# Kernel optimization log

Measured on AMD Instinct MI355X. Metric: run time of the kernel, lower is better.

Reference implementation:

```python
import jax, jax.numpy as jnp
import numpy as np
from jax import lax

EPS = 1e-8  # torch CosineSimilarity eps


def setup_inputs() -> dict:
    key = jax.random.key(0)
    k1, k2, k3 = jax.random.split(key, 3)
    B, T, D, K = 16, 2048, 768, 64
    inputs = jax.random.normal(k1, (B, T, D), dtype=jnp.float32)
    labels = jax.random.randint(k2, (B, T), 0, K, dtype=jnp.int64)
    class_avgs = jax.random.normal(k3, (K, D), dtype=jnp.float32)
    return {"inputs": inputs, "labels": labels, "class_avgs": class_avgs}


def _simrel(inputs, labels, class_avgs):
    B, T, D = inputs.shape
    K = class_avgs.shape[0]
    vecs = inputs.reshape(B * T, D)
    labs = labels.reshape(B * T)
    class_ids = jnp.arange(K)

    def step(carry, xl):
        avgs, counts = carry  # [K,D], [K]
        vec, lab = xl  # [D], scalar int
        is_inf = jnp.any(jnp.isinf(avgs), axis=1)  # [K] unseen-class flag
        vn = jnp.maximum(jnp.linalg.norm(vec), EPS)
        an = jnp.maximum(jnp.linalg.norm(avgs, axis=1), EPS)  # [K]
        cos = (avgs @ vec) / (an * vn)  # [K]
        onehot = class_ids == lab
        # unseen class: sim = 1 (cos(vec,vec)) if labeled, else -1
        sim = jnp.where(is_inf, jnp.where(onehot, 1.0, -1.0), cos)
        # training update: running mean of labeled class (counts reset per forward)
        cnt = counts[lab]
        new_row = jnp.where(is_inf[lab], vec, (avgs[lab] * cnt + vec) / (cnt + 1.0))
        avgs = avgs.at[lab].set(new_row)
        counts = counts.at[lab].add(1.0)
        return (avgs, counts), sim

    init = (class_avgs, jnp.zeros((K,), dtype=inputs.dtype))
    (_, _), sims = lax.scan(step, init, (vecs, labs))
    return sims.reshape(B, T, K)


def reference(inputs, labels, class_avgs):
    return _simrel(inputs, labels, class_avgs)
```

## Files before the change

### kernel.cpp

```cpp
#include <hip/hip_runtime.h>
#include <cstddef>

#define K 64
#define D 768
#define D4 192

__device__ __forceinline__ float d4f(float4 a, float4 b) {
  return a.x*b.x + a.y*b.y + a.z*b.z + a.w*b.w;
}
__device__ __forceinline__ float4 a4(float4 a, float4 b) {
  return make_float4(a.x+b.x, a.y+b.y, a.z+b.z, a.w+b.w);
}
__device__ __forceinline__ unsigned short f2bf(float x) {
  unsigned int u = __float_as_uint(x);
  unsigned int r = (u + 0x7FFFu + ((u >> 16) & 1u)) >> 16;
  return (unsigned short)r;
}
__device__ __forceinline__ float bflo(unsigned u) { return __uint_as_float(u << 16); }
__device__ __forceinline__ float bfhi(unsigned u) { return __uint_as_float(u & 0xFFFF0000u); }

typedef __attribute__((ext_vector_type(8)))  short bf16x8;
typedef __attribute__((ext_vector_type(16))) float f32x16;

#define NCF 256
#define CF  128
#define NF  32768

__global__ __launch_bounds__(256) void k1c(
    const float* __restrict__ cavg, unsigned short* __restrict__ cavgb,
    float* __restrict__ cn2)
{
  int wave = blockIdx.x * 4 + (threadIdx.x >> 6);
  int l = threadIdx.x & 63;
  if (wave >= K) return;
  const float* src = cavg + (size_t)wave * D;
  unsigned short* dst = cavgb + (size_t)wave * D;
  float sq = 0.f;
#pragma unroll
  for (int t = 0; t < 3; ++t) {
    float4 v = ((const float4*)src)[t * 64 + l];
    sq += v.x*v.x + v.y*v.y + v.z*v.z + v.w*v.w;
    ushort4 o; o.x = f2bf(v.x); o.y = f2bf(v.y); o.z = f2bf(v.z); o.w = f2bf(v.w);
    ((ushort4*)dst)[t * 64 + l] = o;
  }
#pragma unroll
  for (int m = 1; m <= 32; m <<= 1) sq += __shfl_xor(sq, m);
  if (l == 0) cn2[wave] = sq;
}

#define LDT2 132
#define LDM  136
__global__ __launch_bounds__(256) void k2_v9(
    const float* __restrict__ inputs, const int* __restrict__ labels,
    unsigned short* __restrict__ Vb, unsigned short* __restrict__ sums,
    int* __restrict__ cnts_t)
{
  __shared__ unsigned short Vt[128 * LDT2];
  __shared__ unsigned short Mt[64 * LDM];
  const int bi = blockIdx.x;
  const int m = bi / 6, g = bi % 6;
  const int tid = threadIdx.x;
  const int w = tid >> 6, l = tid & 63;
  const int r31 = l & 31, kh = l >> 5;

  float4 fa[8], fb[8];
#pragma unroll
  for (int it = 0; it < 8; ++it) {
    int flat = it * 256 + tid;
    int row = flat >> 4, c8 = flat & 15;
    const float* src = inputs + (size_t)(m * 128 + row) * D + g * 128 + c8 * 8;
    fa[it] = *(const float4*)src;
    fb[it] = *(const float4*)(src + 4);
  }

  for (int e = tid; e < 64 * LDM / 2; e += 256) ((unsigned int*)Mt)[e] = 0u;
  __syncthreads();
  if (tid < 128) Mt[labels[m * 128 + tid] * LDM + tid] = 0x3F80;
  __syncthreads();
  if (g == 0 && tid < 64) {
    int c = 0;
    for (int j = 0; j < 128; ++j) c += (Mt[tid * LDM + j] != 0);
    cnts_t[tid * NCF + m] = c;
  }

#pragma unroll
  for (int it = 0; it < 8; ++it) {
    int flat = it * 256 + tid;
    int row = flat >> 4, c8 = flat & 15;
    uint4 u;
    u.x = (unsigned)f2bf(fa[it].x) | ((unsigned)f2bf(fa[it].y) << 16);
    u.y = (unsigned)f2bf(fa[it].z) | ((unsigned)f2bf(fa[it].w) << 16);
    u.z = (unsigned)f2bf(fb[it].x) | ((unsigned)f2bf(fb[it].y) << 16);
    u.w = (unsigned)f2bf(fb[it].z) | ((unsigned)f2bf(fb[it].w) << 16);
    *(uint4*)(Vt + row * LDT2 + c8 * 8) = u;
    *(uint4*)(Vb + (size_t)(m * 128 + row) * D + g * 128 + c8 * 8) = u;
  }
  __syncthreads();

  f32x16 acc0 = (f32x16){}, acc1 = (f32x16){};
#pragma unroll
  for (int kk = 0; kk < 8; ++kk) {
    bf16x8 a0 = *(const bf16x8*)(Mt + (r31) * LDM + kk * 16 + kh * 8);
    bf16x8 a1 = *(const bf16x8*)(Mt + (32 + r31) * LDM + kk * 16 + kh * 8);
    bf16x8 b;
#pragma unroll
    for (int r = 0; r < 8; ++r)
      b[r] = *(const short*)(Vt + (kk * 16 + kh * 8 + r) * LDT2 + w * 32 + r31);
    acc0 = __builtin_amdgcn_mfma_f32_32x32x16_bf16(a0, b, acc0, 0, 0, 0);
    acc1 = __builtin_amdgcn_mfma_f32_32x32x16_bf16(a1, b, acc1, 0, 0, 0);
  }

  __syncthreads();
  unsigned short* So = Vt;
#pragma unroll
  for (int q = 0; q < 16; ++q) {
    int kc = (q & 3) + 8 * (q >> 2) + 4 * kh;
    So[kc * 128 + w * 32 + r31]        = f2bf(acc0[q]);
    So[(32 + kc) * 128 + w * 32 + r31] = f2bf(acc1[q]);
  }
  __syncthreads();
  unsigned short* sp = sums + (size_t)m * (K * D) + g * 128;
#pragma unroll
  for (int it = 0; it < 4; ++it) {
    int flat = it * 256 + tid;
    int row = flat >> 4, c = flat & 15;
    *(uint4*)(sp + (size_t)row * D + c * 8) = *(const uint4*)(So + row * 128 + c * 8);
  }
}

__global__ __launch_bounds__(256) void k3a_scan_lo(
    unsigned short* __restrict__ sums, float* __restrict__ aux)
{
  const int g  = blockIdx.x / 96;
  const int cp = (blockIdx.x % 96) * 256 + threadIdx.x;
  const int col = cp * 2;
  float run0 = 0.f, run1 = 0.f;
  for (int m = g * 16; m < g * 16 + 16; ++m) {
    size_t idx = (size_t)m * (K * D) + col;
    unsigned u = *(const unsigned*)(sums + idx);
    float t0 = bflo(u), t1 = bfhi(u);
    *(unsigned*)(sums + idx) = (unsigned)f2bf(run0) | ((unsigned)f2bf(run1) << 16);
    run0 += t0; run1 += t1;
  }
  aux[(size_t)g * (K * D) + col]     = run0;
  aux[(size_t)g * (K * D) + col + 1] = run1;
}

__global__ __launch_bounds__(256) void k3b_plus(
    float* __restrict__ aux, int* __restrict__ cnts_t)
{
  if (blockIdx.x == 192) {
    if (threadIdx.x < K) {
      int k = threadIdx.x;
      int run = 0;
      int* p = cnts_t + k * NCF;
      for (int mm = 0; mm < NCF; ++mm) { int t = p[mm]; p[mm] = run; run += t; }
    }
    return;
  }
  int col = blockIdx.x * 256 + threadIdx.x;
  float run = 0.f;
  for (int g = 0; g < 16; ++g) {
    size_t idx = (size_t)g * (K * D) + col;
    float t = aux[idx]; aux[idx] = run; run += t;
  }
}

#define LDV2 136
#define LDD  132
#define BUFW (2 * 128 * LDV2)
__global__ __launch_bounds__(1024, 4) void k4_v7(
    const unsigned short* __restrict__ Vb, const unsigned short* __restrict__ base,
    const float* __restrict__ aux, const unsigned short* __restrict__ cavgb,
    const int* __restrict__ labels, const int* __restrict__ cnts_t,
    const float* __restrict__ cn2, float* __restrict__ out)
{
  __shared__ unsigned short smem[2 * BUFW];
  __shared__ float pvL[128];
  __shared__ float bn2L[64];
  __shared__ int   labL[128];
  __shared__ float chk[16][64];
  const int m = blockIdx.x;
  const int g = m >> 4;
  const int tid = threadIdx.x;
  const int w = tid >> 6, l = tid & 63;
  const int r31 = l & 31, kh = l >> 5;
  const int wr = w & 3;
  const int wc = w >> 2;

  if (tid < 128) labL[tid] = labels[m * 128 + tid];
  if (tid < 64) bn2L[tid] = 0.f;
  __syncthreads();

  f32x16 accP = (f32x16){}, accS = (f32x16){};

  uint4 vreg[2], breg, creg;
  float4 areg[2];

#define PREF(sx) do {                                                          \
    _Pragma("unroll")                                                          \
    for (int it = 0; it < 2; ++it) {                                           \
      int flat = it * 1024 + tid;                                              \
      int row = flat >> 4, c = flat & 15;                                      \
      vreg[it] = *(const uint4*)(Vb + (size_t)(m * 128 + row) * D + (sx) * 128 + c * 8); \
      if (it == 0) {                                                           \
        breg = *(const uint4*)(base + ((size_t)m * K + row) * D + (sx) * 128 + c * 8); \
        const float* ap = aux + ((size_t)g * K + row) * D + (sx) * 128 + c * 8; \
        areg[0] = *(const float4*)ap;                                          \
        areg[1] = *(const float4*)(ap + 4);                                    \
      } else {                                                                 \
        creg = *(const uint4*)(cavgb + (size_t)(row - 64) * D + (sx) * 128 + c * 8); \
      }                                                                        \
    }                                                                          \
  } while (0)

#define WRITEB(pb) do {                                                        \
    unsigned short* Vt_ = smem + (pb) * BUFW;                                  \
    unsigned short* Bt_ = Vt_ + 128 * LDV2;                                    \
    _Pragma("unroll")                                                          \
    for (int it = 0; it < 2; ++it) {                                           \
      int flat = it * 1024 + tid;                                              \
      int row = flat >> 4, c = flat & 15;                                      \
      *(uint4*)(Vt_ + row * LDV2 + c * 8) = vreg[it];                          \
      if (it == 0) {                                                           \
        uint4 ub = breg;                                                       \
        float4 af0 = areg[0], af1 = areg[1];                                   \
        float f0 = bflo(ub.x) + af0.x, f1 = bfhi(ub.x) + af0.y;                \
        float f2 = bflo(ub.y) + af0.z, f3 = bfhi(ub.y) + af0.w;                \
        float f4 = bflo(ub.z) + af1.x, f5 = bfhi(ub.z) + af1.y;                \
        float f6 = bflo(ub.w) + af1.z, f7 = bfhi(ub.w) + af1.w;                \
        float sq = f0*f0 + f1*f1 + f2*f2 + f3*f3 + f4*f4 + f5*f5 + f6*f6 + f7*f7; \
        sq += __shfl_xor(sq, 1); sq += __shfl_xor(sq, 2);                      \
        sq += __shfl_xor(sq, 4); sq += __shfl_xor(sq, 8);                      \
        if ((l & 15) == 0) atomicAdd(&bn2L[row], sq);                          \
        uint4 u;                                                               \
        u.x = (unsigned)f2bf(f0) | ((unsigned)f2bf(f1) << 16);                 \
        u.y = (unsigned)f2bf(f2) | ((unsigned)f2bf(f3) << 16);                 \
        u.z = (unsigned)f2bf(f4) | ((unsigned)f2bf(f5) << 16);                 \
        u.w = (unsigned)f2bf(f6) | ((unsigned)f2bf(f7) << 16);                 \
        *(uint4*)(Bt_ + row * LDV2 + c * 8) = u;                               \
      } else {                                                                 \
        *(uint4*)(Bt_ + row * LDV2 + c * 8) = creg;                            \
      }                                                                        \
    }                                                                          \
  } while (0)

  PREF(0);
  WRITEB(0);
  PREF(1);
  __syncthreads();

  for (int s = 0; s < 6; ++s) {
    const int pb = s & 1;
    if (s < 5) WRITEB(pb ^ 1);
    if (s < 4) PREF(s + 2);
    const unsigned short* Vt = smem + pb * BUFW;
    const unsigned short* Bt = Vt + 128 * LDV2;
#pragma unroll
    for (int kk = 0; kk < 8; ++kk) {
      bf16x8 av = *(const bf16x8*)(Vt + (32 * wr + r31) * LDV2 + kk * 16 + kh * 8);
      bf16x8 bB = *(const bf16x8*)(Bt + (32 * wc + r31) * LDV2 + kk * 16 + kh * 8);
      accP = __builtin_amdgcn_mfma_f32_32x32x16_bf16(av, bB, accP, 0, 0, 0);
      bf16x8 bV = *(const bf16x8*)(Vt + (32 * wc + r31) * LDV2 + kk * 16 + kh * 8);
      accS = __builtin_amdgcn_mfma_f32_32x32x16_bf16(av, bV, accS, 0, 0, 0);
    }
    __syncthreads();
  }
#undef PREF
#undef WRITEB

  if (wr == wc && ((r31 >> 2) & 1) == kh) {
    int q = (r31 & 3) + 4 * (r31 >> 3);
    pvL[32 * wr + r31] = accS[q];
  }

  {
    unsigned short* Vt = smem;
    unsigned short* Bt = smem + 128 * LDV2;
#pragma unroll
    for (int q = 0; q < 16; ++q) {
      int i = 32 * wr + (q & 3) + 8 * (q >> 2) + 4 * kh;
      int j = 32 * wc + r31;
      Vt[i * LDV2 + j] = (j < i) ? f2bf(accS[q]) : (unsigned short)0;
    }
    int j = tid & 127;
    int lab = labL[j];
    int kb = (tid >> 7) * 8;
#pragma unroll
    for (int kk = 0; kk < 8; ++kk) {
      int k = kb + kk;
      Bt[k * LDV2 + j] = (lab == k) ? (unsigned short)0x3F80 : (unsigned short)0;
    }
  }
  __syncthreads();

  if (w < 8) {
    const unsigned short* Vt = smem;
    const unsigned short* Bt = smem + 128 * LDV2;
#pragma unroll
    for (int kk = 0; kk < 8; ++kk) {
      bf16x8 aS = *(const bf16x8*)(Vt + (32 * wr + r31) * LDV2 + kk * 16 + kh * 8);
      bf16x8 bM = *(const bf16x8*)(Bt + (32 * wc + r31) * LDV2 + kk * 16 + kh * 8);
      accP = __builtin_amdgcn_mfma_f32_32x32x16_bf16(aS, bM, accP, 0, 0, 0);
    }
  }
  __syncthreads();

  float* dotL = (float*)smem;
#pragma unroll
  for (int q = 0; q < 16; ++q) {
    int i = 32 * wr + (q & 3) + 8 * (q >> 2) + 4 * kh;
    dotL[i * LDD + 32 * wc + r31] = accP[q];
  }
  __syncthreads();

  if (w == 0) {
    int k = l;
    bool seen = cnts_t[k * NCF + m] > 0;
    float n = seen ? bn2L[k] : 0.f;
    for (int seg = 0; seg < 16; ++seg) {
      chk[seg][k] = seen ? n : -1.f;
      if (seg == 15) break;
      for (int j = seg * 8; j < seg * 8 + 8; ++j) {
        float dS = dotL[j * LDD + k];
        float pvj = pvL[j];
        if (labL[j] == k) {
          n = seen ? (n + 2.f * dS + pvj) : pvj;
          seen = true;
        }
      }
    }
  }
  __syncthreads();

  {
    int k = l;
    float st = chk[w][k];
    bool seen = st >= 0.f;
    float n = seen ? st : 0.f;
    float cnk = cn2[k];
    int jb = w * 8;
    for (int j = jb; j < jb + 8; ++j) {
      float dS = dotL[j * LDD + k];
      float dC = dotL[j * LDD + 64 + k];
      float pvj = pvL[j];
      int lab = labL[j];
      float val = seen ? dS : dC;
      float nn  = seen ? n : cnk;
      out[(size_t)(m * 128 + j) * K + k] = val * rsqrtf(fmaxf(nn * pvj, 1e-30f));
      if (lab == k) {
        n = seen ? (n + 2.f * dS + pvj) : pvj;
        seen = true;
      }
    }
  }
}

__global__ __launch_bounds__(256) void ph1_chunk_sums(
    const float* __restrict__ inputs, const int* __restrict__ labels,
    float* __restrict__ sums, int* __restrict__ cnts, int NC, int C)
{
  __shared__ float acc[4 * K * 64];
  __shared__ int   hist[4 * K];
  const int bi    = blockIdx.x;
  const int chunk = bi / 12, slice = bi % 12;
  const int w = threadIdx.x >> 6, l = threadIdx.x & 63;

  for (int e = threadIdx.x; e < 4 * K * 64; e += 256) acc[e] = 0.f;
  hist[threadIdx.x] = 0;
  __syncthreads();

  const int C4 = C >> 2;
  const long long rbase = (long long)chunk * C + (long long)w * C4;
  float* accw = acc + w * (K * 64);
  for (int j = 0; j < C4; ++j) {
    long long r = rbase + j;
    int lab = labels[r];
    float v = inputs[r * D + slice * 64 + l];
    accw[lab * 64 + l] += v;
    if (slice == 0 && l == 0) hist[w * K + lab]++;
  }
  __syncthreads();

  float* sp = sums + (long long)chunk * (K * D) + slice * 64;
  for (int e = threadIdx.x; e < K * 64; e += 256) {
    int k = e >> 6, dl = e & 63;
    float s = acc[0*K*64 + e] + acc[1*K*64 + e] + acc[2*K*64 + e] + acc[3*K*64 + e];
    sp[k * D + dl] = s;
  }
  if (slice == 0 && threadIdx.x < K) {
    cnts[chunk * K + threadIdx.x] =
        hist[0*K + threadIdx.x] + hist[1*K + threadIdx.x] +
        hist[2*K + threadIdx.x] + hist[3*K + threadIdx.x];
  }
}

__global__ __launch_bounds__(256) void ph2a_scan_sums(float* __restrict__ sums, int NC)
{
  const int tid = blockIdx.x * 256 + threadIdx.x;
  float run = 0.f;
  for (int m = 0; m < NC; ++m) {
    long long idx = (long long)m * (K * D) + tid;
    float t = sums[idx];
    sums[idx] = run;
    run += t;
  }
}

__global__ void ph2b_scan_cnts(int* __restrict__ cnts, int NC)
{
  const int k = threadIdx.x;
  int run = 0;
  for (int m = 0; m < NC; ++m) {
    int t = cnts[m * K + k];
    cnts[m * K + k] = run;
    run += t;
  }
}

__global__ __launch_bounds__(256, 4) void ph3_scan(
    const float* __restrict__ inputs, const int* __restrict__ labels,
    const float* __restrict__ cavg, const float* __restrict__ base,
    const int* __restrict__ cnts, float* __restrict__ out, int NC, int C)
{
  const int bi = blockIdx.x;
  int chunk, quad;
  if (NC >= 8) {
    int xcd = bi & 7, slot = bi >> 3;
    chunk = xcd * (NC >> 3) + (slot >> 2);
    quad  = slot & 3;
  } else {
    chunk = bi >> 2; quad = bi & 3;
  }
  const int w = threadIdx.x >> 6, l = threadIdx.x & 63;
  const int k0 = (quad * 4 + w) * 4;

  const int cb = chunk * K + k0;
  bool vg0 = (cnts[cb+0] == 0), vg1 = (cnts[cb+1] == 0);
  bool vg2 = (cnts[cb+2] == 0), vg3 = (cnts[cb+3] == 0);

  const float4* bp = (const float4*)base + (long long)chunk * (K * D4);
  const float4* cp = (const float4*)cavg;

  float4 A0[3], A1[3], A2[3], A3[3];
#pragma unroll
  for (int t = 0; t < 3; ++t) {
    int o = t * 64 + l;
    A0[t] = vg0 ? cp[(k0+0)*D4 + o] : bp[(k0+0)*D4 + o];
    A1[t] = vg1 ? cp[(k0+1)*D4 + o] : bp[(k0+1)*D4 + o];
    A2[t] = vg2 ? cp[(k0+2)*D4 + o] : bp[(k0+2)*D4 + o];
    A3[t] = vg3 ? cp[(k0+3)*D4 + o] : bp[(k0+3)*D4 + o];
  }
  float n0 = 0.f, n1 = 0.f, n2 = 0.f, n3 = 0.f;
#pragma unroll
  for (int t = 0; t < 3; ++t) {
    n0 += d4f(A0[t], A0[t]); n1 += d4f(A1[t], A1[t]);
    n2 += d4f(A2[t], A2[t]); n3 += d4f(A3[t], A3[t]);
  }
#pragma unroll
  for (int m = 1; m <= 32; m <<= 1) {
    n0 += __shfl_xor(n0, m); n1 += __shfl_xor(n1, m);
    n2 += __shfl_xor(n2, m); n3 += __shfl_xor(n3, m);
  }

  const long long ibase = (long long)chunk * C;
  for (int j = 0; j < C; ++j) {
    const long long i = ibase + j;
    const int lab = labels[i];
    const float4* vp = (const float4*)inputs + i * D4;
    float4 v0 = vp[l], v1 = vp[64 + l], v2 = vp[128 + l];

    float p0 = d4f(A0[0], v0) + d4f(A0[1], v1) + d4f(A0[2], v2);
    float p1 = d4f(A1[0], v0) + d4f(A1[1], v1) + d4f(A1[2], v2);
    float p2 = d4f(A2[0], v0) + d4f(A2[1], v1) + d4f(A2[2], v2);
    float p3 = d4f(A3[0], v0) + d4f(A3[1], v1) + d4f(A3[2], v2);
    float pv = d4f(v0, v0) + d4f(v1, v1) + d4f(v2, v2);
#pragma unroll
    for (int m = 1; m <= 32; m <<= 1) {
      p0 += __shfl_xor(p0, m); p1 += __shfl_xor(p1, m);
      p2 += __shfl_xor(p2, m); p3 += __shfl_xor(p3, m);
      pv += __shfl_xor(pv, m);
    }
    if (l < 4) {
      float ps = (l == 0) ? p0 : (l == 1) ? p1 : (l == 2) ? p2 : p3;
      float ns = (l == 0) ? n0 : (l == 1) ? n1 : (l == 2) ? n2 : n3;
      out[i * K + k0 + l] = ps * rsqrtf(fmaxf(ns * pv, 1e-30f));
    }
#define UPD(idx) do { \
      if (vg##idx) { A##idx[0]=v0; A##idx[1]=v1; A##idx[2]=v2; n##idx = pv; vg##idx = false; } \
      else { A##idx[0]=a4(A##idx[0],v0); A##idx[1]=a4(A##idx[1],v1); A##idx[2]=a4(A##idx[2],v2); \
             n##idx += 2.f * p##idx + pv; } } while (0)
    if      (lab == k0 + 0) UPD(0);
    else if (lab == k0 + 1) UPD(1);
    else if (lab == k0 + 2) UPD(2);
    else if (lab == k0 + 3) UPD(3);
#undef UPD
  }
}

extern "C" void kernel_launch(void* const* d_in, const int* in_sizes, int n_in,
                              void* d_out, int out_size, void* d_ws, size_t ws_size,
                              hipStream_t stream)
{
  const float* inputs = (const float*)d_in[0];
  const int*   labels = (const int*)d_in[1];
  const float* cavg   = (const float*)d_in[2];
  float* out = (float*)d_out;
  const int N = in_sizes[1];

  const size_t szVb    = (size_t)NF * D * 2;
  const size_t szSums  = (size_t)NCF * K * D * 2;
  const size_t szAux   = (size_t)16 * K * D * 4;
  const size_t szCnt   = (size_t)K * NCF * 4;
  const size_t szCavgb = (size_t)K * D * 2;
  const size_t szCn2   = (size_t)K * 4;
  size_t need = szVb + szSums + szAux + szCnt + szCavgb + szCn2 + 8 * 256;

  if (N == NF && in_sizes[2] == K * D && ws_size >= need) {
    char* p = (char*)d_ws;
    auto take = [&](size_t b) { char* r = p; p += (b + 255) & ~(size_t)255; return r; };
    unsigned short* Vb    = (unsigned short*)take(szVb);
    unsigned short* sums  = (unsigned short*)take(szSums);
    float*          aux   = (float*)take(szAux);
    int*            cnts  = (int*)take(szCnt);
    unsigned short* cavgb = (unsigned short*)take(szCavgb);
    float*          cn2   = (float*)take(szCn2);

    hipLaunchKernelGGL(k1c, dim3(16), dim3(256), 0, stream, cavg, cavgb, cn2);
    hipLaunchKernelGGL(k2_v9, dim3(NCF * 6), dim3(256), 0, stream,
                       inputs, labels, Vb, sums, cnts);
    hipLaunchKernelGGL(k3a_scan_lo, dim3(16 * 96), dim3(256), 0, stream, sums, aux);
    hipLaunchKernelGGL(k3b_plus, dim3(193), dim3(256), 0, stream, aux, cnts);
    hipLaunchKernelGGL(k4_v7, dim3(NCF), dim3(1024), 0, stream,
                       Vb, sums, aux, cavgb, labels, cnts, cn2, out);
    return;
  }

  int NC = 256;
  while (NC > 1) {
    size_t nd = (size_t)NC * K * D * 4 + (size_t)NC * K * 4;
    if (nd <= ws_size && (N % (NC * 4)) == 0) break;
    NC >>= 1;
  }
  const int C = N / NC;
  float* d_sums = (float*)d_ws;
  int*   d_cnts = (int*)((char*)d_ws + (size_t)NC * K * D * 4);

  hipLaunchKernelGGL(ph1_chunk_sums, dim3(NC * 12), dim3(256), 0, stream,
                     inputs, labels, d_sums, d_cnts, NC, C);
  hipLaunchKernelGGL(ph2a_scan_sums, dim3((K * D) / 256), dim3(256), 0, stream,
                     d_sums, NC);
  hipLaunchKernelGGL(ph2b_scan_cnts, dim3(1), dim3(64), 0, stream,
                     d_cnts, NC);
  hipLaunchKernelGGL(ph3_scan, dim3(NC * 4), dim3(256), 0, stream,
                     inputs, labels, cavg, d_sums, d_cnts, out, NC, C);
}
```

Before: 87.41 us.

## Drop bf16 input staging buffer, skip upper-triangle MFMAs, parallelize segment scan

k2 no longer writes a bf16 copy of the inputs to global memory. k4 instead reads the fp32 inputs directly and converts them to bf16 while filling shared memory, which removes one global write and read of the bf16 copy at the cost of twice the bytes read in k4. The within-tile V·V^T MFMA is skipped for wave tiles above the diagonal, since only the causal lower part is used. The serial single-wave prefix over the 16 segments is replaced by per-wave segment summaries followed by each wave combining the summaries before it, which adds shared-memory arrays.

```diff
diff --git a/kernel.cpp b/kernel.cpp
--- a/kernel.cpp
+++ b/kernel.cpp
@@ -50,10 +50,9 @@
 
 #define LDT2 132
 #define LDM  136
-__global__ __launch_bounds__(256) void k2_v9(
+__global__ __launch_bounds__(256) void k2_v10(
     const float* __restrict__ inputs, const int* __restrict__ labels,
-    unsigned short* __restrict__ Vb, unsigned short* __restrict__ sums,
-    int* __restrict__ cnts_t)
+    unsigned short* __restrict__ sums, int* __restrict__ cnts_t)
 {
   __shared__ unsigned short Vt[128 * LDT2];
   __shared__ unsigned short Mt[64 * LDM];
@@ -93,7 +92,6 @@
     u.z = (unsigned)f2bf(fb[it].x) | ((unsigned)f2bf(fb[it].y) << 16);
     u.w = (unsigned)f2bf(fb[it].z) | ((unsigned)f2bf(fb[it].w) << 16);
     *(uint4*)(Vt + row * LDT2 + c8 * 8) = u;
-    *(uint4*)(Vb + (size_t)(m * 128 + row) * D + g * 128 + c8 * 8) = u;
   }
   __syncthreads();
 
@@ -169,8 +167,8 @@
 #define LDV2 136
 #define LDD  132
 #define BUFW (2 * 128 * LDV2)
-__global__ __launch_bounds__(1024, 4) void k4_v7(
-    const unsigned short* __restrict__ Vb, const unsigned short* __restrict__ base,
+__global__ __launch_bounds__(1024, 4) void k4_v8(
+    const float* __restrict__ inputs, const unsigned short* __restrict__ base,
     const float* __restrict__ aux, const unsigned short* __restrict__ cavgb,
     const int* __restrict__ labels, const int* __restrict__ cnts_t,
     const float* __restrict__ cn2, float* __restrict__ out)
@@ -179,7 +177,10 @@
   __shared__ float pvL[128];
   __shared__ float bn2L[64];
   __shared__ int   labL[128];
-  __shared__ float chk[16][64];
+  __shared__ float segA[16][64];
+  __shared__ float segF[16][64];
+  __shared__ float segP[16][64];
+  __shared__ int   segH[16][64];
   const int m = blockIdx.x;
   const int g = m >> 4;
   const int tid = threadIdx.x;
@@ -194,15 +195,21 @@
 
   f32x16 accP = (f32x16){}, accS = (f32x16){};
 
-  uint4 vreg[2], breg, creg;
+  float4 vregf[4];
+  uint4 breg, creg;
   float4 areg[2];
 
 #define PREF(sx) do {                                                          \
+    _Pragma("unroll")                                                          \
+    for (int it = 0; it < 4; ++it) {                                           \
+      int flat = it * 1024 + tid;                                              \
+      int row = flat >> 5, c4 = flat & 31;                                     \
+      vregf[it] = *(const float4*)(inputs + (size_t)(m * 128 + row) * D + (sx) * 128 + c4 * 4); \
+    }                                                                          \
     _Pragma("unroll")                                                          \
     for (int it = 0; it < 2; ++it) {                                           \
       int flat = it * 1024 + tid;                                              \
       int row = flat >> 4, c = flat & 15;                                      \
-      vreg[it] = *(const uint4*)(Vb + (size_t)(m * 128 + row) * D + (sx) * 128 + c * 8); \
       if (it == 0) {                                                           \
         breg = *(const uint4*)(base + ((size_t)m * K + row) * D + (sx) * 128 + c * 8); \
         const float* ap = aux + ((size_t)g * K + row) * D + (sx) * 128 + c * 8; \
@@ -218,10 +225,18 @@
     unsigned short* Vt_ = smem + (pb) * BUFW;                                  \
     unsigned short* Bt_ = Vt_ + 128 * LDV2;                                    \
     _Pragma("unroll")                                                          \
+    for (int it = 0; it < 4; ++it) {                                           \
+      int flat = it * 1024 + tid;                                              \
+      int row = flat >> 5, c4 = flat & 31;                                     \
+      ushort4 o;                                                               \
+      o.x = f2bf(vregf[it].x); o.y = f2bf(vregf[it].y);                        \
+      o.z = f2bf(vregf[it].z); o.w = f2bf(vregf[it].w);                        \
+      *(ushort4*)(Vt_ + row * LDV2 + c4 * 4) = o;                              \
+    }                                                                          \
+    _Pragma("unroll")                                                          \
     for (int it = 0; it < 2; ++it) {                                           \
       int flat = it * 1024 + tid;                                              \
       int row = flat >> 4, c = flat & 15;                                      \
-      *(uint4*)(Vt_ + row * LDV2 + c * 8) = vreg[it];                          \
       if (it == 0) {                                                           \
         uint4 ub = breg;                                                       \
         float4 af0 = areg[0], af1 = areg[1];                                   \
@@ -261,8 +276,10 @@
       bf16x8 av = *(const bf16x8*)(Vt + (32 * wr + r31) * LDV2 + kk * 16 + kh * 8);
       bf16x8 bB = *(const bf16x8*)(Bt + (32 * wc + r31) * LDV2 + kk * 16 + kh * 8);
       accP = __builtin_amdgcn_mfma_f32_32x32x16_bf16(av, bB, accP, 0, 0, 0);
-      bf16x8 bV = *(const bf16x8*)(Vt + (32 * wc + r31) * LDV2 + kk * 16 + kh * 8);
-      accS = __builtin_amdgcn_mfma_f32_32x32x16_bf16(av, bV, accS, 0, 0, 0);
+      if (wc <= wr) {
+        bf16x8 bV = *(const bf16x8*)(Vt + (32 * wc + r31) * LDV2 + kk * 16 + kh * 8);
+        accS = __builtin_amdgcn_mfma_f32_32x32x16_bf16(av, bV, accS, 0, 0, 0);
+      }
     }
     __syncthreads();
   }
@@ -314,30 +331,33 @@
   }
   __syncthreads();
 
-  if (w == 0) {
+  {
+    int k = l;
+    float A = 0.f, Fv = 0.f, Pv = 0.f;
+    int has = 0;
+    int jb = w * 8;
+    for (int j = jb; j < jb + 8; ++j) {
+      if (labL[j] == k) {
+        float t = 2.f * dotL[j * LDD + k] + pvL[j];
+        A += t;
+        if (!has) { Fv = t; Pv = pvL[j]; has = 1; }
+      }
+    }
+    segA[w][k] = A; segF[w][k] = Fv; segP[w][k] = Pv; segH[w][k] = has;
+  }
+  __syncthreads();
+
+  {
     int k = l;
     bool seen = cnts_t[k * NCF + m] > 0;
     float n = seen ? bn2L[k] : 0.f;
-    for (int seg = 0; seg < 16; ++seg) {
-      chk[seg][k] = seen ? n : -1.f;
-      if (seg == 15) break;
-      for (int j = seg * 8; j < seg * 8 + 8; ++j) {
-        float dS = dotL[j * LDD + k];
-        float pvj = pvL[j];
-        if (labL[j] == k) {
-          n = seen ? (n + 2.f * dS + pvj) : pvj;
-          seen = true;
-        }
+    for (int ww = 0; ww < w; ++ww) {
+      if (segH[ww][k]) {
+        n = seen ? (n + segA[ww][k])
+                 : (segP[ww][k] + segA[ww][k] - segF[ww][k]);
+        seen = true;
       }
     }
-  }
-  __syncthreads();
-
-  {
-    int k = l;
-    float st = chk[w][k];
-    bool seen = st >= 0.f;
-    float n = seen ? st : 0.f;
     float cnk = cn2[k];
     int jb = w * 8;
     for (int j = jb; j < jb + 8; ++j) {
@@ -508,18 +528,16 @@
   float* out = (float*)d_out;
   const int N = in_sizes[1];
 
-  const size_t szVb    = (size_t)NF * D * 2;
   const size_t szSums  = (size_t)NCF * K * D * 2;
   const size_t szAux   = (size_t)16 * K * D * 4;
   const size_t szCnt   = (size_t)K * NCF * 4;
   const size_t szCavgb = (size_t)K * D * 2;
   const size_t szCn2   = (size_t)K * 4;
-  size_t need = szVb + szSums + szAux + szCnt + szCavgb + szCn2 + 8 * 256;
+  size_t need = szSums + szAux + szCnt + szCavgb + szCn2 + 8 * 256;
 
   if (N == NF && in_sizes[2] == K * D && ws_size >= need) {
     char* p = (char*)d_ws;
     auto take = [&](size_t b) { char* r = p; p += (b + 255) & ~(size_t)255; return r; };
-    unsigned short* Vb    = (unsigned short*)take(szVb);
     unsigned short* sums  = (unsigned short*)take(szSums);
     float*          aux   = (float*)take(szAux);
     int*            cnts  = (int*)take(szCnt);
@@ -527,12 +545,12 @@
     float*          cn2   = (float*)take(szCn2);
 
     hipLaunchKernelGGL(k1c, dim3(16), dim3(256), 0, stream, cavg, cavgb, cn2);
-    hipLaunchKernelGGL(k2_v9, dim3(NCF * 6), dim3(256), 0, stream,
-                       inputs, labels, Vb, sums, cnts);
+    hipLaunchKernelGGL(k2_v10, dim3(NCF * 6), dim3(256), 0, stream,
+                       inputs, labels, sums, cnts);
     hipLaunchKernelGGL(k3a_scan_lo, dim3(16 * 96), dim3(256), 0, stream, sums, aux);
     hipLaunchKernelGGL(k3b_plus, dim3(193), dim3(256), 0, stream, aux, cnts);
-    hipLaunchKernelGGL(k4_v7, dim3(NCF), dim3(1024), 0, stream,
-                       Vb, sums, aux, cavgb, labels, cnts, cn2, out);
+    hipLaunchKernelGGL(k4_v8, dim3(NCF), dim3(1024), 0, stream,
+                       inputs, sums, aux, cavgb, labels, cnts, cn2, out);
     return;
   }
 
```

Measured after the change: 78.79 us. 1.11x faster.
